# Performance work log

Hardware: AMD Instinct MI355X
Metric: run time of the kernel (lower is better)

Reference implementation:

```python
import jax, jax.numpy as jnp
import numpy as np

B, D, H, T = 8192, 256, 266, 20  # batch, dim, dim+10, num timesteps
LAMBDA = 1.0
SIGMA = 1.0
EPS = 1e-5  # torch BatchNorm1d default eps


def _bn(h, g, b):
    # training-mode BatchNorm1d: biased batch statistics over axis 0
    m = h.mean(0)
    v = h.var(0)
    return g * (h - m) * jax.lax.rsqrt(v + EPS) + b


def _hidden(x, W, b, g, be):
    return jax.nn.relu(_bn(x @ W.T + b, g, be))


def setup_inputs() -> dict:
    key = jax.random.key(0)
    ks = jax.random.split(key, 16)

    def n(k, shape, s=0.05):
        return jax.random.normal(k, shape, jnp.float32) * s

    inp = {}
    inp["x"] = jax.random.normal(ks[0], (B, D), jnp.float32)
    inp["xi"] = jax.random.normal(ks[1], (T, B, D), jnp.float32)
    inp["timegrid"] = jnp.linspace(0.0, 1.0, T + 1).astype(jnp.float32)
    # per-timestep stacks of Linear+BN params (i_h1, h1_h2, h2_o)
    inp["W1"] = n(ks[2], (T, H, D)); inp["b1"] = jnp.zeros((T, H), jnp.float32)
    inp["g1"] = jnp.ones((T, H), jnp.float32); inp["be1"] = jnp.zeros((T, H), jnp.float32)
    inp["W2"] = n(ks[3], (T, H, H)); inp["b2"] = jnp.zeros((T, H), jnp.float32)
    inp["g2"] = jnp.ones((T, H), jnp.float32); inp["be2"] = jnp.zeros((T, H), jnp.float32)
    inp["W3"] = n(ks[4], (T, D, H)); inp["b3"] = jnp.zeros((T, D), jnp.float32)
    # v0 network: hiddenLayer(D,H) -> hiddenLayer(H,H) -> hiddenLayer(H,1)
    inp["vW1"] = n(ks[5], (H, D)); inp["vb1"] = jnp.zeros((H,), jnp.float32)
    inp["vg1"] = jnp.ones((H,), jnp.float32); inp["vbe1"] = jnp.zeros((H,), jnp.float32)
    inp["vW2"] = n(ks[6], (H, H)); inp["vb2"] = jnp.zeros((H,), jnp.float32)
    inp["vg2"] = jnp.ones((H,), jnp.float32); inp["vbe2"] = jnp.zeros((H,), jnp.float32)
    inp["vW3"] = n(ks[7], (1, H)); inp["vb3"] = jnp.zeros((1,), jnp.float32)
    inp["vg3"] = jnp.ones((1,), jnp.float32); inp["vbe3"] = jnp.zeros((1,), jnp.float32)
    return inp


def reference(x, xi, timegrid, W1, b1, g1, be1, W2, b2, g2, be2, W3, b3,
              vW1, vb1, vg1, vbe1, vW2, vb2, vg2, vbe2, vW3, vb3, vg3, vbe3):
    # v0 sub-network evaluated on the initial x (i == 0 branch)
    v0 = _hidden(x, vW1, vb1, vg1, vbe1)
    v0 = _hidden(v0, vW2, vb2, vg2, vbe2)
    v0 = _hidden(v0, vW3, vb3, vg3, vbe3)  # [B, 1]

    hsteps = timegrid[1:] - timegrid[:-1]  # [T]

    def step(carry, inp_t):
        xt, vt = carry
        (W1t, b1t, g1t, be1t, W2t, b2t, g2t, be2t, W3t, b3t, ht, xit) = inp_t
        h1 = _hidden(xt, W1t, b1t, g1t, be1t)
        h2 = _hidden(h1, W2t, b2t, g2t, be2t)
        grad = h2 @ W3t.T + b3t                     # [B, D]
        alpha = -jnp.sqrt(LAMBDA) * grad
        f = jnp.sum(alpha * alpha, axis=1)          # ||alpha||_2^2 per row
        noise = SIGMA * jnp.sqrt(ht) * xit          # sigma*sqrt(h)*xi
        # diag(grad @ noise.T) == row-wise dot product (same math, O(B*D))
        dot = jnp.sum(grad * noise, axis=1)
        vt = vt - (f * ht)[:, None] + dot[:, None]
        xt = xt + alpha * ht + noise
        return (xt, vt), None

    (xT, vT), _ = jax.lax.scan(
        step, (x, v0),
        (W1, b1, g1, be1, W2, b2, g2, be2, W3, b3, hsteps, xi))
    return vT, xT
```

## Files before the change

kernel.cpp:

```cpp
#include <hip/hip_runtime.h>
#include <hip/hip_bf16.h>
#include <math.h>

#define BATCH 8192
#define DDIM 256
#define HDIM 266
#define NPAD 320
#define TSTEPS 20
#define BN_EPS 1e-5f
#define LSTR 72

typedef __attribute__((ext_vector_type(8))) short short8;
typedef __attribute__((ext_vector_type(4))) float f32x4;

__device__ __forceinline__ short f2bf(float f) {
    __hip_bfloat16 h = __float2bfloat16(f);
    return *reinterpret_cast<short*>(&h);
}
__device__ __forceinline__ float bf2f(short s) {
    union { unsigned u; float f; } v;
    v.u = ((unsigned)(unsigned short)s) << 16;
    return v.f;
}

#define SZ_W1B (20L * 320 * 256)
#define SZ_W2B (20L * 320 * 320)
#define SZ_W3B (20L * 256 * 320)
#define SZ_VW1 (320L * 256)
#define SZ_VW2 (320L * 320)
#define SZ_B1P (20L * 320)
#define SZ_B2P (20L * 320)
#define PREP_TOTAL (SZ_W1B + SZ_W2B + SZ_W3B + SZ_VW1 + SZ_VW2 + SZ_B1P + SZ_B2P + 3 * 320)

__global__ __launch_bounds__(256)
void prep_k(short* __restrict__ W1b, const float* __restrict__ W1,
            short* __restrict__ W2b, const float* __restrict__ W2,
            short* __restrict__ W3b, const float* __restrict__ W3,
            short* __restrict__ vW1b, const float* __restrict__ vW1,
            short* __restrict__ vW2b, const float* __restrict__ vW2,
            float* __restrict__ b1p, const float* __restrict__ b1,
            float* __restrict__ b2p, const float* __restrict__ b2,
            float* __restrict__ vb1p, const float* __restrict__ vb1,
            float* __restrict__ vb2p, const float* __restrict__ vb2,
            float* __restrict__ vW3p, const float* __restrict__ vW3)
{
    long idx = (long)blockIdx.x * 256 + threadIdx.x;
    if (idx < SZ_W1B) {
        long k = idx % 256, r = (idx / 256) % 320, t = idx / (256L * 320);
        float v = (r < HDIM) ? W1[((size_t)t * HDIM + r) * 256 + k] : 0.0f;
        W1b[idx] = f2bf(v); return;
    }
    idx -= SZ_W1B;
    if (idx < SZ_W2B) {
        long k = idx % 320, r = (idx / 320) % 320, t = idx / (320L * 320);
        float v = (r < HDIM && k < HDIM) ? W2[((size_t)t * HDIM + r) * HDIM + k] : 0.0f;
        W2b[idx] = f2bf(v); return;
    }
    idx -= SZ_W2B;
    if (idx < SZ_W3B) {
        long k = idx % 320, r = (idx / 320) % 256, t = idx / (320L * 256);
        float v = (k < HDIM) ? W3[((size_t)t * 256 + r) * HDIM + k] : 0.0f;
        W3b[idx] = f2bf(v); return;
    }
    idx -= SZ_W3B;
    if (idx < SZ_VW1) {
        long k = idx % 256, r = idx / 256;
        float v = (r < HDIM) ? vW1[(size_t)r * 256 + k] : 0.0f;
        vW1b[idx] = f2bf(v); return;
    }
    idx -= SZ_VW1;
    if (idx < SZ_VW2) {
        long k = idx % 320, r = idx / 320;
        float v = (r < HDIM && k < HDIM) ? vW2[(size_t)r * HDIM + k] : 0.0f;
        vW2b[idx] = f2bf(v); return;
    }
    idx -= SZ_VW2;
    if (idx < SZ_B1P) { long n = idx % 320, t = idx / 320;
        b1p[idx] = (n < HDIM) ? b1[(size_t)t * HDIM + n] : 0.0f; return; }
    idx -= SZ_B1P;
    if (idx < SZ_B2P) { long n = idx % 320, t = idx / 320;
        b2p[idx] = (n < HDIM) ? b2[(size_t)t * HDIM + n] : 0.0f; return; }
    idx -= SZ_B2P;
    if (idx < 320) { vb1p[idx] = (idx < HDIM) ? vb1[idx] : 0.0f; return; }
    idx -= 320;
    if (idx < 320) { vb2p[idx] = (idx < HDIM) ? vb2[idx] : 0.0f; return; }
    idx -= 320;
    if (idx < 320) { vW3p[idx] = (idx < HDIM) ? vW3[idx] : 0.0f; return; }
}

__global__ __launch_bounds__(256)
void init_k(const float* __restrict__ x, short* __restrict__ xtb,
            float* __restrict__ zbase, int zcount)
{
    int i = blockIdx.x * 256 + threadIdx.x;
    if (i < BATCH * DDIM) xtb[i] = f2bf(x[i]);
    if (i < zcount) zbase[i] = 0.0f;
}

__global__ __launch_bounds__(256)
void gemm1_k(const short* __restrict__ A, const short* __restrict__ W,
             const float* __restrict__ biasp, short* __restrict__ C,
             float* __restrict__ csum, float* __restrict__ csq)
{
    __shared__ __align__(16) short As[64 * LSTR];
    __shared__ __align__(16) short Bs[64 * LSTR];
    const int tid = threadIdx.x;
    const int col0 = blockIdx.x * 64, row0 = blockIdx.y * 64;
    const int lane = tid & 63, w = tid >> 6, q = lane >> 4, m = lane & 15;
    const int wr = (w >> 1) * 32, wc = (w & 1) * 32;
    const int srow = tid >> 2, kq = (tid & 3) * 8;

    const short* ap = A + (size_t)(row0 + srow) * DDIM + kq;
    const short* wp = W + (size_t)(col0 + srow) * DDIM + kq;
    short8 ra0 = *(const short8*)ap;
    short8 ra1 = *(const short8*)(ap + 32);
    short8 rw0 = *(const short8*)wp;
    short8 rw1 = *(const short8*)(wp + 32);

    f32x4 acc[2][2];
    #pragma unroll
    for (int i = 0; i < 2; ++i)
        #pragma unroll
        for (int j = 0; j < 2; ++j) acc[i][j] = (f32x4){0.f, 0.f, 0.f, 0.f};

    #pragma unroll
    for (int kt = 0; kt < 4; ++kt) {
        *(short8*)&As[srow * LSTR + kq]      = ra0;
        *(short8*)&As[srow * LSTR + kq + 32] = ra1;
        *(short8*)&Bs[srow * LSTR + kq]      = rw0;
        *(short8*)&Bs[srow * LSTR + kq + 32] = rw1;
        __syncthreads();
        if (kt < 3) {
            ap += 64; wp += 64;
            ra0 = *(const short8*)ap; ra1 = *(const short8*)(ap + 32);
            rw0 = *(const short8*)wp; rw1 = *(const short8*)(wp + 32);
        }
        #pragma unroll
        for (int kk = 0; kk < 2; ++kk) {
            short8 fa0 = *(const short8*)&As[(wr + m)      * LSTR + kk * 32 + q * 8];
            short8 fa1 = *(const short8*)&As[(wr + 16 + m) * LSTR + kk * 32 + q * 8];
            short8 fb0 = *(const short8*)&Bs[(wc + m)      * LSTR + kk * 32 + q * 8];
            short8 fb1 = *(const short8*)&Bs[(wc + 16 + m) * LSTR + kk * 32 + q * 8];
            acc[0][0] = __builtin_amdgcn_mfma_f32_16x16x32_bf16(fa0, fb0, acc[0][0], 0, 0, 0);
            acc[0][1] = __builtin_amdgcn_mfma_f32_16x16x32_bf16(fa0, fb1, acc[0][1], 0, 0, 0);
            acc[1][0] = __builtin_amdgcn_mfma_f32_16x16x32_bf16(fa1, fb0, acc[1][0], 0, 0, 0);
            acc[1][1] = __builtin_amdgcn_mfma_f32_16x16x32_bf16(fa1, fb1, acc[1][1], 0, 0, 0);
        }
        __syncthreads();
    }

    float cs[2], cq[2];
    #pragma unroll
    for (int j = 0; j < 2; ++j) {
        const int col = col0 + wc + j * 16 + m;
        const float bv = biasp[col];
        float s = 0.0f, sq = 0.0f;
        #pragma unroll
        for (int i = 0; i < 2; ++i)
            #pragma unroll
            for (int r = 0; r < 4; ++r) {
                float v = acc[i][j][r] + bv;
                int row = row0 + wr + i * 16 + q * 4 + r;
                C[(size_t)row * NPAD + col] = f2bf(v);
                s += v; sq += v * v;
            }
        cs[j] = s; cq[j] = sq;
    }
    #pragma unroll
    for (int j = 0; j < 2; ++j) {
        cs[j] += __shfl_xor(cs[j], 16); cs[j] += __shfl_xor(cs[j], 32);
        cq[j] += __shfl_xor(cq[j], 16); cq[j] += __shfl_xor(cq[j], 32);
    }
    float* reds = (float*)As;
    float* redq = (float*)Bs;
    if (q == 0) {
        #pragma unroll
        for (int j = 0; j < 2; ++j) {
            reds[(w >> 1) * 64 + wc + j * 16 + m] = cs[j];
            redq[(w >> 1) * 64 + wc + j * 16 + m] = cq[j];
        }
    }
    __syncthreads();
    if (tid < 64) {
        int col = col0 + tid;
        if (col < HDIM) {
            atomicAdd(&csum[col], reds[tid] + reds[64 + tid]);
            atomicAdd(&csq[col],  redq[tid] + redq[64 + tid]);
        }
    }
}

__global__ __launch_bounds__(256)
void gemm2_k(const short* __restrict__ A, const short* __restrict__ W,
             const float* __restrict__ biasp,
             const float* __restrict__ csum_in, const float* __restrict__ csq_in,
             const float* __restrict__ g, const float* __restrict__ be,
             short* __restrict__ C,
             float* __restrict__ csum_out, float* __restrict__ csq_out)
{
    __shared__ __align__(16) short As[32 * LSTR];
    __shared__ __align__(16) short Bs[160 * LSTR];
    __shared__ float sS[NPAD], sT[NPAD];
    const int tid = threadIdx.x;
    for (int k = tid; k < NPAD; k += 256) {
        float s = 0.0f, t = 0.0f;
        if (k < HDIM) {
            float mn = csum_in[k] * (1.0f / BATCH);
            float vr = csq_in[k] * (1.0f / BATCH) - mn * mn;
            float rs = rsqrtf(fmaxf(vr, 0.0f) + BN_EPS);
            s = g[k] * rs;
            t = be[k] - mn * s;
        }
        sS[k] = s; sT[k] = t;
    }
    __syncthreads();

    const int col0 = blockIdx.x * 160, row0 = blockIdx.y * 32;
    const int lane = tid & 63, w = tid >> 6, q = lane >> 4, m = lane & 15;
    const int rh = w >> 1, ch = w & 1;
    const int srowA = tid >> 3, kqA = (tid & 7) * 8;

    const short* ap = A + (size_t)(row0 + srowA) * NPAD + kqA;
    short8 rA = *(const short8*)ap;
    short8 rB[5];
    #pragma unroll
    for (int i = 0; i < 5; ++i) {
        int s = tid + 256 * i;
        rB[i] = *(const short8*)(W + (size_t)(col0 + (s >> 3)) * NPAD + ((s & 7) * 8));
    }

    f32x4 acc[5];
    #pragma unroll
    for (int j = 0; j < 5; ++j) acc[j] = (f32x4){0.f, 0.f, 0.f, 0.f};

    #pragma unroll
    for (int kt = 0; kt < 5; ++kt) {
        short8 ta;
        const int kb = kt * 64 + kqA;
        #pragma unroll
        for (int j = 0; j < 8; ++j) {
            float f = bf2f(rA[j]);
            f = fmaxf(f * sS[kb + j] + sT[kb + j], 0.0f);
            ta[j] = f2bf(f);
        }
        *(short8*)&As[srowA * LSTR + kqA] = ta;
        #pragma unroll
        for (int i = 0; i < 5; ++i) {
            int s = tid + 256 * i;
            *(short8*)&Bs[(s >> 3) * LSTR + (s & 7) * 8] = rB[i];
        }
        __syncthreads();
        if (kt < 4) {
            ap += 64;
            rA = *(const short8*)ap;
            #pragma unroll
            for (int i = 0; i < 5; ++i) {
                int s = tid + 256 * i;
                rB[i] = *(const short8*)(W + (size_t)(col0 + (s >> 3)) * NPAD
                                         + (kt + 1) * 64 + ((s & 7) * 8));
            }
        }
        #pragma unroll
        for (int kk = 0; kk < 2; ++kk) {
            short8 fa = *(const short8*)&As[(rh * 16 + m) * LSTR + kk * 32 + q * 8];
            #pragma unroll
            for (int j = 0; j < 5; ++j) {
                short8 fb = *(const short8*)&Bs[(ch * 80 + j * 16 + m) * LSTR + kk * 32 + q * 8];
                acc[j] = __builtin_amdgcn_mfma_f32_16x16x32_bf16(fa, fb, acc[j], 0, 0, 0);
            }
        }
        __syncthreads();
    }

    float csv[5], cqv[5];
    #pragma unroll
    for (int j = 0; j < 5; ++j) {
        const int col = col0 + ch * 80 + j * 16 + m;
        const float bv = biasp[col];
        float s = 0.0f, sq = 0.0f;
        #pragma unroll
        for (int r = 0; r < 4; ++r) {
            float v = acc[j][r] + bv;
            int row = row0 + rh * 16 + q * 4 + r;
            C[(size_t)row * NPAD + col] = f2bf(v);
            s += v; sq += v * v;
        }
        csv[j] = s; cqv[j] = sq;
    }
    #pragma unroll
    for (int j = 0; j < 5; ++j) {
        csv[j] += __shfl_xor(csv[j], 16); csv[j] += __shfl_xor(csv[j], 32);
        cqv[j] += __shfl_xor(cqv[j], 16); cqv[j] += __shfl_xor(cqv[j], 32);
    }
    float* redS = (float*)As;
    float* redQ = redS + 320;
    if (q == 0) {
        #pragma unroll
        for (int j = 0; j < 5; ++j) {
            redS[rh * 160 + ch * 80 + j * 16 + m] = csv[j];
            redQ[rh * 160 + ch * 80 + j * 16 + m] = cqv[j];
        }
    }
    __syncthreads();
    if (tid < 160) {
        int col = col0 + tid;
        if (col < HDIM) {
            atomicAdd(&csum_out[col], redS[tid] + redS[160 + tid]);
            atomicAdd(&csq_out[col],  redQ[tid] + redQ[160 + tid]);
        }
    }
}

__global__ __launch_bounds__(256)
void gemm3_k(const short* __restrict__ A, const short* __restrict__ W,
             const float* __restrict__ bias,
             const float* __restrict__ csum_in, const float* __restrict__ csq_in,
             const float* __restrict__ g, const float* __restrict__ be,
             const float* __restrict__ xi_t,
             short* __restrict__ xtb, float* __restrict__ xout,
             float* __restrict__ ftab, float* __restrict__ dtab,
             const float* __restrict__ tg, int t, int last)
{
    __shared__ __align__(16) short As[32 * LSTR];
    __shared__ __align__(16) short Bs[128 * LSTR];
    __shared__ float sS[NPAD], sT[NPAD];
    const int tid = threadIdx.x;
    for (int k = tid; k < NPAD; k += 256) {
        float s = 0.0f, tt = 0.0f;
        if (k < HDIM) {
            float mn = csum_in[k] * (1.0f / BATCH);
            float vr = csq_in[k] * (1.0f / BATCH) - mn * mn;
            float rs = rsqrtf(fmaxf(vr, 0.0f) + BN_EPS);
            s = g[k] * rs;
            tt = be[k] - mn * s;
        }
        sS[k] = s; sT[k] = tt;
    }
    __syncthreads();

    const int col0 = blockIdx.x * 128, row0 = blockIdx.y * 32;
    const int lane = tid & 63, w = tid >> 6, q = lane >> 4, m = lane & 15;
    const int rh = w >> 1, ch = w & 1;
    const int srowA = tid >> 3, kqA = (tid & 7) * 8;

    const short* ap = A + (size_t)(row0 + srowA) * NPAD + kqA;
    short8 rA = *(const short8*)ap;
    short8 rB[4];
    #pragma unroll
    for (int i = 0; i < 4; ++i) {
        int s = tid + 256 * i;
        rB[i] = *(const short8*)(W + (size_t)(col0 + (s >> 3)) * NPAD + ((s & 7) * 8));
    }

    f32x4 acc[4];
    #pragma unroll
    for (int j = 0; j < 4; ++j) acc[j] = (f32x4){0.f, 0.f, 0.f, 0.f};

    #pragma unroll
    for (int kt = 0; kt < 5; ++kt) {
        short8 ta;
        const int kb = kt * 64 + kqA;
        #pragma unroll
        for (int j = 0; j < 8; ++j) {
            float f = bf2f(rA[j]);
            f = fmaxf(f * sS[kb + j] + sT[kb + j], 0.0f);
            ta[j] = f2bf(f);
        }
        *(short8*)&As[srowA * LSTR + kqA] = ta;
        #pragma unroll
        for (int i = 0; i < 4; ++i) {
            int s = tid + 256 * i;
            *(short8*)&Bs[(s >> 3) * LSTR + (s & 7) * 8] = rB[i];
        }
        __syncthreads();
        if (kt < 4) {
            ap += 64;
            rA = *(const short8*)ap;
            #pragma unroll
            for (int i = 0; i < 4; ++i) {
                int s = tid + 256 * i;
                rB[i] = *(const short8*)(W + (size_t)(col0 + (s >> 3)) * NPAD
                                         + (kt + 1) * 64 + ((s & 7) * 8));
            }
        }
        #pragma unroll
        for (int kk = 0; kk < 2; ++kk) {
            short8 fa = *(const short8*)&As[(rh * 16 + m) * LSTR + kk * 32 + q * 8];
            #pragma unroll
            for (int j = 0; j < 4; ++j) {
                short8 fb = *(const short8*)&Bs[(ch * 64 + j * 16 + m) * LSTR + kk * 32 + q * 8];
                acc[j] = __builtin_amdgcn_mfma_f32_16x16x32_bf16(fa, fb, acc[j], 0, 0, 0);
            }
        }
        __syncthreads();
    }

    const float ht = tg[t + 1] - tg[t];
    const float sn = sqrtf(ht);
    float fr[4] = {0.f, 0.f, 0.f, 0.f};
    float dr[4] = {0.f, 0.f, 0.f, 0.f};
    #pragma unroll
    for (int j = 0; j < 4; ++j) {
        const int col = col0 + ch * 64 + j * 16 + m;
        const float bv = bias[col];
        #pragma unroll
        for (int r = 0; r < 4; ++r) {
            const int row = row0 + rh * 16 + q * 4 + r;
            size_t idx = (size_t)row * DDIM + col;
            float grad = acc[j][r] + bv;
            float noise = sn * xi_t[idx];
            float nx = bf2f(xtb[idx]) - grad * ht + noise;
            xtb[idx] = f2bf(nx);
            if (last) xout[idx] = nx;
            fr[r] += grad * grad;
            dr[r] += grad * noise;
        }
    }
    #pragma unroll
    for (int r = 0; r < 4; ++r) {
        fr[r] += __shfl_xor(fr[r], 1); dr[r] += __shfl_xor(dr[r], 1);
        fr[r] += __shfl_xor(fr[r], 2); dr[r] += __shfl_xor(dr[r], 2);
        fr[r] += __shfl_xor(fr[r], 4); dr[r] += __shfl_xor(dr[r], 4);
        fr[r] += __shfl_xor(fr[r], 8); dr[r] += __shfl_xor(dr[r], 8);
    }
    if (m == 0) {
        #pragma unroll
        for (int r = 0; r < 4; ++r) {
            const int row = row0 + rh * 16 + q * 4 + r;
            atomicAdd(&ftab[row], fr[r]);
            atomicAdd(&dtab[row], dr[r]);
        }
    }
}

__global__ __launch_bounds__(256)
void vrow_k(const short* __restrict__ A,
            const float* __restrict__ csum_in, const float* __restrict__ csq_in,
            const float* __restrict__ g, const float* __restrict__ be,
            const float* __restrict__ vW3p, const float* __restrict__ vb3,
            float* __restrict__ pre3, float* __restrict__ s3, float* __restrict__ q3)
{
    __shared__ float sS[NPAD], sT[NPAD];
    __shared__ float wred[8];
    const int tid = threadIdx.x;
    for (int k = tid; k < NPAD; k += 256) {
        float s = 0.0f, t = 0.0f;
        if (k < HDIM) {
            float mn = csum_in[k] * (1.0f / BATCH);
            float vr = csq_in[k] * (1.0f / BATCH) - mn * mn;
            float rs = rsqrtf(fmaxf(vr, 0.0f) + BN_EPS);
            s = g[k] * rs;
            t = be[k] - mn * s;
        }
        sS[k] = s; sT[k] = t;
    }
    __syncthreads();
    const int wave = tid >> 6, lane = tid & 63;
    const int row = blockIdx.x * 4 + wave;
    float sum = 0.0f;
    #pragma unroll
    for (int c = 0; c < 5; ++c) {
        int k = c * 64 + lane;
        float v = fmaxf(bf2f(A[(size_t)row * NPAD + k]) * sS[k] + sT[k], 0.0f);
        sum += v * vW3p[k];
    }
    sum += __shfl_xor(sum, 1);  sum += __shfl_xor(sum, 2);
    sum += __shfl_xor(sum, 4);  sum += __shfl_xor(sum, 8);
    sum += __shfl_xor(sum, 16); sum += __shfl_xor(sum, 32);
    if (lane == 0) {
        float p = sum + vb3[0];
        pre3[row] = p;
        wred[wave] = p;
        wred[4 + wave] = p * p;
    }
    __syncthreads();
    if (tid == 0) {
        atomicAdd(s3, wred[0] + wred[1] + wred[2] + wred[3]);
        atomicAdd(q3, wred[4] + wred[5] + wred[6] + wred[7]);
    }
}

__global__ __launch_bounds__(256)
void v3b_k(const float* __restrict__ pre3,
           const float* __restrict__ s3, const float* __restrict__ q3,
           const float* __restrict__ vg3, const float* __restrict__ vbe3,
           float* __restrict__ vt)
{
    int i = blockIdx.x * 256 + threadIdx.x;
    float mn = s3[0] * (1.0f / BATCH);
    float va = fmaxf(q3[0] * (1.0f / BATCH) - mn * mn, 0.0f);
    float rs = rsqrtf(va + BN_EPS);
    if (i < BATCH) vt[i] = fmaxf(vg3[0] * (pre3[i] - mn) * rs + vbe3[0], 0.0f);
}

__global__ __launch_bounds__(256)
void final_v_k(const float* __restrict__ vt,
               const float* __restrict__ ftab, const float* __restrict__ dtab,
               const float* __restrict__ tg, float* __restrict__ outv)
{
    int i = blockIdx.x * 256 + threadIdx.x;
    if (i >= BATCH) return;
    float v = vt[i];
    for (int t = 0; t < TSTEPS; ++t) {
        float ht = tg[t + 1] - tg[t];
        v += dtab[(size_t)t * BATCH + i] - ftab[(size_t)t * BATCH + i] * ht;
    }
    outv[i] = v;
}

extern "C" void kernel_launch(void* const* d_in, const int* in_sizes, int n_in,
                              void* d_out, int out_size, void* d_ws, size_t ws_size,
                              hipStream_t stream)
{
    const float* x    = (const float*)d_in[0];
    const float* xi   = (const float*)d_in[1];
    const float* tg   = (const float*)d_in[2];
    const float* W1   = (const float*)d_in[3];
    const float* b1   = (const float*)d_in[4];
    const float* g1   = (const float*)d_in[5];
    const float* be1  = (const float*)d_in[6];
    const float* W2   = (const float*)d_in[7];
    const float* b2   = (const float*)d_in[8];
    const float* g2   = (const float*)d_in[9];
    const float* be2  = (const float*)d_in[10];
    const float* W3   = (const float*)d_in[11];
    const float* b3   = (const float*)d_in[12];
    const float* vW1  = (const float*)d_in[13];
    const float* vb1  = (const float*)d_in[14];
    const float* vg1  = (const float*)d_in[15];
    const float* vbe1 = (const float*)d_in[16];
    const float* vW2  = (const float*)d_in[17];
    const float* vb2  = (const float*)d_in[18];
    const float* vg2  = (const float*)d_in[19];
    const float* vbe2 = (const float*)d_in[20];
    const float* vW3  = (const float*)d_in[21];
    const float* vb3  = (const float*)d_in[22];
    const float* vg3  = (const float*)d_in[23];
    const float* vbe3 = (const float*)d_in[24];

    float* out  = (float*)d_out;
    float* xout = out + BATCH;

    short* xtb  = (short*)d_ws;
    short* hp1  = xtb + (size_t)BATCH * DDIM;
    short* hp2  = hp1 + (size_t)BATCH * NPAD;
    short* W1b  = hp2 + (size_t)BATCH * NPAD;
    short* W2b  = W1b + SZ_W1B;
    short* W3b  = W2b + SZ_W2B;
    short* vW1b = W3b + SZ_W3B;
    short* vW2b = vW1b + SZ_VW1;
    float* fbase = (float*)(vW2b + SZ_VW2);
    float* b1p  = fbase;
    float* b2p  = b1p + TSTEPS * NPAD;
    float* vb1p = b2p + TSTEPS * NPAD;
    float* vb2p = vb1p + NPAD;
    float* vW3p = vb2p + NPAD;
    float* vt   = vW3p + NPAD;
    float* pre3 = vt + BATCH;
    float* ftab = pre3 + BATCH;
    float* dtab = ftab + (size_t)TSTEPS * BATCH;
    float* csA  = dtab + (size_t)TSTEPS * BATCH;
    float* cqA  = csA + 21 * NPAD;
    float* csB  = cqA + 21 * NPAD;
    float* cqB  = csB + 21 * NPAD;
    float* s3   = cqB + 21 * NPAD;
    float* q3   = s3 + 1;
    const int zcount = 2 * TSTEPS * BATCH + 4 * 21 * NPAD + 2;

    dim3 blk(256);
    dim3 g1g(5, BATCH / 64);
    dim3 g2g(2, BATCH / 32);
    dim3 g3g(2, BATCH / 32);

    init_k<<<dim3((BATCH * DDIM + 255) / 256), blk, 0, stream>>>(x, xtb, ftab, zcount);
    prep_k<<<dim3((int)((PREP_TOTAL + 255) / 256)), blk, 0, stream>>>(
        W1b, W1, W2b, W2, W3b, W3, vW1b, vW1, vW2b, vW2,
        b1p, b1, b2p, b2, vb1p, vb1, vb2p, vb2, vW3p, vW3);

    float* csV1 = csA + 20 * NPAD; float* cqV1 = cqA + 20 * NPAD;
    float* csV2 = csB + 20 * NPAD; float* cqV2 = cqB + 20 * NPAD;
    gemm1_k<<<g1g, blk, 0, stream>>>(xtb, vW1b, vb1p, hp1, csV1, cqV1);
    gemm2_k<<<g2g, blk, 0, stream>>>(hp1, vW2b, vb2p, csV1, cqV1, vg1, vbe1,
                                     hp2, csV2, cqV2);
    vrow_k<<<dim3(BATCH / 4), blk, 0, stream>>>(hp2, csV2, cqV2, vg2, vbe2,
                                                vW3p, vb3, pre3, s3, q3);
    v3b_k<<<dim3(BATCH / 256), blk, 0, stream>>>(pre3, s3, q3, vg3, vbe3, vt);

    for (int t = 0; t < TSTEPS; ++t) {
        gemm1_k<<<g1g, blk, 0, stream>>>(
            xtb, W1b + (size_t)t * NPAD * DDIM, b1p + t * NPAD,
            hp1, csA + t * NPAD, cqA + t * NPAD);
        gemm2_k<<<g2g, blk, 0, stream>>>(
            hp1, W2b + (size_t)t * NPAD * NPAD, b2p + t * NPAD,
            csA + t * NPAD, cqA + t * NPAD, g1 + t * HDIM, be1 + t * HDIM,
            hp2, csB + t * NPAD, cqB + t * NPAD);
        gemm3_k<<<g3g, blk, 0, stream>>>(
            hp2, W3b + (size_t)t * DDIM * NPAD, b3 + t * DDIM,
            csB + t * NPAD, cqB + t * NPAD, g2 + t * HDIM, be2 + t * HDIM,
            xi + (size_t)t * BATCH * DDIM, xtb, xout,
            ftab + (size_t)t * BATCH, dtab + (size_t)t * BATCH,
            tg, t, (t == TSTEPS - 1) ? 1 : 0);
    }
    final_v_k<<<dim3(BATCH / 256), blk, 0, stream>>>(vt, ftab, dtab, tg, out);
}
```

Before: 1.144 ms.

## Fuse next-step first-layer GEMM into output GEMM and batch v0 network launches

Gemm3 now produces full 32-row tiles across all 256 output columns with 512-thread blocks, so each block can immediately run the next timestep's first-layer GEMM on its freshly updated x rows from shared memory. This removes the per-step gemm1 launch and its re-read of xt. The v0 network runs alongside step 0 through a z-dimension of the grid, and init and the v3b work are merged into prep and the final kernel. ftab/dtab are written directly rather than by atomics. The trade-off is larger shared memory and register use per block and fewer blocks in flight (256 blocks), which may lower occupancy.

```diff
diff --git a/kernel.cpp b/kernel.cpp
--- a/kernel.cpp
+++ b/kernel.cpp
@@ -30,7 +30,9 @@
 #define SZ_VW2 (320L * 320)
 #define SZ_B1P (20L * 320)
 #define SZ_B2P (20L * 320)
-#define PREP_TOTAL (SZ_W1B + SZ_W2B + SZ_W3B + SZ_VW1 + SZ_VW2 + SZ_B1P + SZ_B2P + 3 * 320)
+#define SZ_XTB (8192L * 256)
+#define ZCOUNT (4L * 21 * NPAD + 2)
+#define PREP_TOTAL (SZ_W1B + SZ_W2B + SZ_W3B + SZ_VW1 + SZ_VW2 + SZ_B1P + SZ_B2P + 3 * 320 + SZ_XTB + ZCOUNT)
 
 __global__ __launch_bounds__(256)
 void prep_k(short* __restrict__ W1b, const float* __restrict__ W1,
@@ -42,7 +44,9 @@
             float* __restrict__ b2p, const float* __restrict__ b2,
             float* __restrict__ vb1p, const float* __restrict__ vb1,
             float* __restrict__ vb2p, const float* __restrict__ vb2,
-            float* __restrict__ vW3p, const float* __restrict__ vW3)
+            float* __restrict__ vW3p, const float* __restrict__ vW3,
+            const float* __restrict__ x, short* __restrict__ xtb,
+            float* __restrict__ zbase)
 {
     long idx = (long)blockIdx.x * 256 + threadIdx.x;
     if (idx < SZ_W1B) {
@@ -86,22 +90,25 @@
     if (idx < 320) { vb2p[idx] = (idx < HDIM) ? vb2[idx] : 0.0f; return; }
     idx -= 320;
     if (idx < 320) { vW3p[idx] = (idx < HDIM) ? vW3[idx] : 0.0f; return; }
+    idx -= 320;
+    if (idx < SZ_XTB) { xtb[idx] = f2bf(x[idx]); return; }
+    idx -= SZ_XTB;
+    if (idx < ZCOUNT) { zbase[idx] = 0.0f; return; }
 }
 
 __global__ __launch_bounds__(256)
-void init_k(const float* __restrict__ x, short* __restrict__ xtb,
-            float* __restrict__ zbase, int zcount)
+void gemm1_k(const short* __restrict__ A,
+             const short* __restrict__ W0a, const float* __restrict__ bias0,
+             short* __restrict__ C0a, float* __restrict__ cs0, float* __restrict__ cq0,
+             const short* __restrict__ W1a, const float* __restrict__ bias1,
+             short* __restrict__ C1a, float* __restrict__ cs1, float* __restrict__ cq1)
 {
-    int i = blockIdx.x * 256 + threadIdx.x;
-    if (i < BATCH * DDIM) xtb[i] = f2bf(x[i]);
-    if (i < zcount) zbase[i] = 0.0f;
-}
-
-__global__ __launch_bounds__(256)
-void gemm1_k(const short* __restrict__ A, const short* __restrict__ W,
-             const float* __restrict__ biasp, short* __restrict__ C,
-             float* __restrict__ csum, float* __restrict__ csq)
-{
+    const short* W      = blockIdx.z ? W1a   : W0a;
+    const float* biasp  = blockIdx.z ? bias1 : bias0;
+    short* C            = blockIdx.z ? C1a   : C0a;
+    float* csum         = blockIdx.z ? cs1   : cs0;
+    float* csq          = blockIdx.z ? cq1   : cq0;
+
     __shared__ __align__(16) short As[64 * LSTR];
     __shared__ __align__(16) short Bs[64 * LSTR];
     const int tid = threadIdx.x;
@@ -191,13 +198,28 @@
 }
 
 __global__ __launch_bounds__(256)
-void gemm2_k(const short* __restrict__ A, const short* __restrict__ W,
-             const float* __restrict__ biasp,
-             const float* __restrict__ csum_in, const float* __restrict__ csq_in,
-             const float* __restrict__ g, const float* __restrict__ be,
-             short* __restrict__ C,
-             float* __restrict__ csum_out, float* __restrict__ csq_out)
+void gemm2_k(const short* __restrict__ A0a, const short* __restrict__ W0a,
+             const float* __restrict__ bias0,
+             const float* __restrict__ csi0, const float* __restrict__ cqi0,
+             const float* __restrict__ g0a, const float* __restrict__ be0a,
+             short* __restrict__ C0a, float* __restrict__ cso0, float* __restrict__ cqo0,
+             const short* __restrict__ A1a, const short* __restrict__ W1a,
+             const float* __restrict__ bias1,
+             const float* __restrict__ csi1, const float* __restrict__ cqi1,
+             const float* __restrict__ g1a, const float* __restrict__ be1a,
+             short* __restrict__ C1a, float* __restrict__ cso1, float* __restrict__ cqo1)
 {
+    const short* A       = blockIdx.z ? A1a   : A0a;
+    const short* W       = blockIdx.z ? W1a   : W0a;
+    const float* biasp   = blockIdx.z ? bias1 : bias0;
+    const float* csum_in = blockIdx.z ? csi1  : csi0;
+    const float* csq_in  = blockIdx.z ? cqi1  : cqi0;
+    const float* g       = blockIdx.z ? g1a   : g0a;
+    const float* be      = blockIdx.z ? be1a  : be0a;
+    short* C             = blockIdx.z ? C1a   : C0a;
+    float* csum_out      = blockIdx.z ? cso1  : cso0;
+    float* csq_out       = blockIdx.z ? cqo1  : cqo0;
+
     __shared__ __align__(16) short As[32 * LSTR];
     __shared__ __align__(16) short Bs[160 * LSTR];
     __shared__ float sS[NPAD], sT[NPAD];
@@ -311,21 +333,78 @@
     }
 }
 
-__global__ __launch_bounds__(256)
-void gemm3_k(const short* __restrict__ A, const short* __restrict__ W,
-             const float* __restrict__ bias,
-             const float* __restrict__ csum_in, const float* __restrict__ csq_in,
-             const float* __restrict__ g, const float* __restrict__ be,
-             const float* __restrict__ xi_t,
-             short* __restrict__ xtb, float* __restrict__ xout,
-             float* __restrict__ ftab, float* __restrict__ dtab,
-             const float* __restrict__ tg, int t, int last)
+__global__ __launch_bounds__(512)
+void g31_k(const short* __restrict__ A,
+           const short* __restrict__ W3t, const float* __restrict__ b3t,
+           const float* __restrict__ csum_in, const float* __restrict__ csq_in,
+           const float* __restrict__ g, const float* __restrict__ be,
+           const float* __restrict__ xi_t,
+           short* __restrict__ xtb, float* __restrict__ xout,
+           float* __restrict__ ftab_t, float* __restrict__ dtab_t,
+           const float* __restrict__ tg, int t, int last,
+           const short* __restrict__ W1n, const float* __restrict__ b1n,
+           short* __restrict__ hp1, float* __restrict__ csn, float* __restrict__ cqn,
+           const short* __restrict__ Av, const float* __restrict__ csV, const float* __restrict__ cqV,
+           const float* __restrict__ vg, const float* __restrict__ vbe,
+           const float* __restrict__ vW3p, const float* __restrict__ vb3,
+           float* __restrict__ pre3, float* __restrict__ s3, float* __restrict__ q3)
 {
-    __shared__ __align__(16) short As[32 * LSTR];
-    __shared__ __align__(16) short Bs[128 * LSTR];
+    __shared__ __align__(16) short As1[32 * LSTR];
+    __shared__ __align__(16) short As2[128 * LSTR];
+    __shared__ __align__(16) short Bs[320 * LSTR];
     __shared__ float sS[NPAD], sT[NPAD];
+    __shared__ float redF[128], redD[128];
+    __shared__ float redS[2 * NPAD], redQ[2 * NPAD];
+
     const int tid = threadIdx.x;
-    for (int k = tid; k < NPAD; k += 256) {
+    const int row0 = blockIdx.x * 32;
+
+    if (blockIdx.z == 1) {
+        for (int k = tid; k < NPAD; k += 512) {
+            float s = 0.0f, tt = 0.0f;
+            if (k < HDIM) {
+                float mn = csV[k] * (1.0f / BATCH);
+                float vr = cqV[k] * (1.0f / BATCH) - mn * mn;
+                float rs = rsqrtf(fmaxf(vr, 0.0f) + BN_EPS);
+                s = vg[k] * rs;
+                tt = vbe[k] - mn * s;
+            }
+            sS[k] = s; sT[k] = tt;
+        }
+        __syncthreads();
+        const int wv = tid >> 6, lane = tid & 63;
+        float ps = 0.0f, pq = 0.0f;
+        #pragma unroll
+        for (int r4 = 0; r4 < 4; ++r4) {
+            int row = row0 + wv * 4 + r4;
+            float sum = 0.0f;
+            #pragma unroll
+            for (int c = 0; c < 5; ++c) {
+                int k = c * 64 + lane;
+                float v = fmaxf(bf2f(Av[(size_t)row * NPAD + k]) * sS[k] + sT[k], 0.0f);
+                sum += v * vW3p[k];
+            }
+            sum += __shfl_xor(sum, 1);  sum += __shfl_xor(sum, 2);
+            sum += __shfl_xor(sum, 4);  sum += __shfl_xor(sum, 8);
+            sum += __shfl_xor(sum, 16); sum += __shfl_xor(sum, 32);
+            if (lane == 0) {
+                float p = sum + vb3[0];
+                pre3[row] = p;
+                ps += p; pq += p * p;
+            }
+        }
+        if (lane == 0) { redF[wv] = ps; redD[wv] = pq; }
+        __syncthreads();
+        if (tid == 0) {
+            float a = 0.0f, b = 0.0f;
+            #pragma unroll
+            for (int i = 0; i < 8; ++i) { a += redF[i]; b += redD[i]; }
+            atomicAdd(s3, a); atomicAdd(q3, b);
+        }
+        return;
+    }
+
+    for (int k = tid; k < NPAD; k += 512) {
         float s = 0.0f, tt = 0.0f;
         if (k < HDIM) {
             float mn = csum_in[k] * (1.0f / BATCH);
@@ -338,18 +417,18 @@
     }
     __syncthreads();
 
-    const int col0 = blockIdx.x * 128, row0 = blockIdx.y * 32;
     const int lane = tid & 63, w = tid >> 6, q = lane >> 4, m = lane & 15;
-    const int rh = w >> 1, ch = w & 1;
+    const int rh = w >> 2, ch = w & 3;
     const int srowA = tid >> 3, kqA = (tid & 7) * 8;
 
     const short* ap = A + (size_t)(row0 + srowA) * NPAD + kqA;
-    short8 rA = *(const short8*)ap;
+    short8 rA;
+    if (tid < 256) rA = *(const short8*)ap;
     short8 rB[4];
     #pragma unroll
     for (int i = 0; i < 4; ++i) {
-        int s = tid + 256 * i;
-        rB[i] = *(const short8*)(W + (size_t)(col0 + (s >> 3)) * NPAD + ((s & 7) * 8));
+        int s = tid + 512 * i;
+        rB[i] = *(const short8*)(W3t + (size_t)(s >> 3) * NPAD + ((s & 7) * 8));
     }
 
     f32x4 acc[4];
@@ -358,34 +437,36 @@
 
     #pragma unroll
     for (int kt = 0; kt < 5; ++kt) {
-        short8 ta;
-        const int kb = kt * 64 + kqA;
-        #pragma unroll
-        for (int j = 0; j < 8; ++j) {
-            float f = bf2f(rA[j]);
-            f = fmaxf(f * sS[kb + j] + sT[kb + j], 0.0f);
-            ta[j] = f2bf(f);
-        }
-        *(short8*)&As[srowA * LSTR + kqA] = ta;
+        if (tid < 256) {
+            short8 ta;
+            const int kb = kt * 64 + kqA;
+            #pragma unroll
+            for (int j = 0; j < 8; ++j) {
+                float f = bf2f(rA[j]);
+                f = fmaxf(f * sS[kb + j] + sT[kb + j], 0.0f);
+                ta[j] = f2bf(f);
+            }
+            *(short8*)&As1[srowA * LSTR + kqA] = ta;
+        }
         #pragma unroll
         for (int i = 0; i < 4; ++i) {
-            int s = tid + 256 * i;
+            int s = tid + 512 * i;
             *(short8*)&Bs[(s >> 3) * LSTR + (s & 7) * 8] = rB[i];
         }
         __syncthreads();
         if (kt < 4) {
             ap += 64;
-            rA = *(const short8*)ap;
+            if (tid < 256) rA = *(const short8*)ap;
             #pragma unroll
             for (int i = 0; i < 4; ++i) {
-                int s = tid + 256 * i;
-                rB[i] = *(const short8*)(W + (size_t)(col0 + (s >> 3)) * NPAD
+                int s = tid + 512 * i;
+                rB[i] = *(const short8*)(W3t + (size_t)(s >> 3) * NPAD
                                          + (kt + 1) * 64 + ((s & 7) * 8));
             }
         }
         #pragma unroll
         for (int kk = 0; kk < 2; ++kk) {
-            short8 fa = *(const short8*)&As[(rh * 16 + m) * LSTR + kk * 32 + q * 8];
+            short8 fa = *(const short8*)&As1[(rh * 16 + m) * LSTR + kk * 32 + q * 8];
             #pragma unroll
             for (int j = 0; j < 4; ++j) {
                 short8 fb = *(const short8*)&Bs[(ch * 64 + j * 16 + m) * LSTR + kk * 32 + q * 8];
@@ -393,6 +474,15 @@
             }
         }
         __syncthreads();
+    }
+
+    short8 rW[5];
+    if (!last) {
+        #pragma unroll
+        for (int i = 0; i < 5; ++i) {
+            int s = tid + 512 * i;
+            rW[i] = *(const short8*)(W1n + (size_t)(s >> 3) * DDIM + ((s & 7) * 8));
+        }
     }
 
     const float ht = tg[t + 1] - tg[t];
@@ -401,17 +491,18 @@
     float dr[4] = {0.f, 0.f, 0.f, 0.f};
     #pragma unroll
     for (int j = 0; j < 4; ++j) {
-        const int col = col0 + ch * 64 + j * 16 + m;
-        const float bv = bias[col];
+        const int col = ch * 64 + j * 16 + m;
+        const float bv = b3t[col];
         #pragma unroll
         for (int r = 0; r < 4; ++r) {
-            const int row = row0 + rh * 16 + q * 4 + r;
-            size_t idx = (size_t)row * DDIM + col;
+            const int lr = rh * 16 + q * 4 + r;
+            const size_t idx = (size_t)(row0 + lr) * DDIM + col;
             float grad = acc[j][r] + bv;
             float noise = sn * xi_t[idx];
             float nx = bf2f(xtb[idx]) - grad * ht + noise;
             xtb[idx] = f2bf(nx);
             if (last) xout[idx] = nx;
+            else      As2[(ch * 32 + lr) * LSTR + (j * 16 + m)] = f2bf(nx);
             fr[r] += grad * grad;
             dr[r] += grad * noise;
         }
@@ -426,81 +517,96 @@
     if (m == 0) {
         #pragma unroll
         for (int r = 0; r < 4; ++r) {
-            const int row = row0 + rh * 16 + q * 4 + r;
-            atomicAdd(&ftab[row], fr[r]);
-            atomicAdd(&dtab[row], dr[r]);
-        }
+            redF[ch * 32 + rh * 16 + q * 4 + r] = fr[r];
+            redD[ch * 32 + rh * 16 + q * 4 + r] = dr[r];
+        }
+    }
+    __syncthreads();
+    if (tid < 32) {
+        ftab_t[row0 + tid] = redF[tid] + redF[32 + tid] + redF[64 + tid] + redF[96 + tid];
+        dtab_t[row0 + tid] = redD[tid] + redD[32 + tid] + redD[64 + tid] + redD[96 + tid];
+    }
+    if (last) return;
+
+    f32x4 acc2[5];
+    #pragma unroll
+    for (int j = 0; j < 5; ++j) acc2[j] = (f32x4){0.f, 0.f, 0.f, 0.f};
+
+    #pragma unroll
+    for (int kt = 0; kt < 4; ++kt) {
+        #pragma unroll
+        for (int i = 0; i < 5; ++i) {
+            int s = tid + 512 * i;
+            *(short8*)&Bs[(s >> 3) * LSTR + (s & 7) * 8] = rW[i];
+        }
+        __syncthreads();
+        if (kt < 3) {
+            #pragma unroll
+            for (int i = 0; i < 5; ++i) {
+                int s = tid + 512 * i;
+                rW[i] = *(const short8*)(W1n + (size_t)(s >> 3) * DDIM
+                                         + (kt + 1) * 64 + ((s & 7) * 8));
+            }
+        }
+        #pragma unroll
+        for (int kk = 0; kk < 2; ++kk) {
+            short8 fa = *(const short8*)&As2[(kt * 32 + rh * 16 + m) * LSTR + kk * 32 + q * 8];
+            #pragma unroll
+            for (int j = 0; j < 5; ++j) {
+                short8 fb = *(const short8*)&Bs[(ch * 80 + j * 16 + m) * LSTR + kk * 32 + q * 8];
+                acc2[j] = __builtin_amdgcn_mfma_f32_16x16x32_bf16(fa, fb, acc2[j], 0, 0, 0);
+            }
+        }
+        __syncthreads();
+    }
+
+    float csv[5], cqv[5];
+    #pragma unroll
+    for (int j = 0; j < 5; ++j) {
+        const int col = ch * 80 + j * 16 + m;
+        const float bv = b1n[col];
+        float s = 0.0f, sq = 0.0f;
+        #pragma unroll
+        for (int r = 0; r < 4; ++r) {
+            float v = acc2[j][r] + bv;
+            int row = row0 + rh * 16 + q * 4 + r;
+            hp1[(size_t)row * NPAD + col] = f2bf(v);
+            s += v; sq += v * v;
+        }
+        csv[j] = s; cqv[j] = sq;
+    }
+    #pragma unroll
+    for (int j = 0; j < 5; ++j) {
+        csv[j] += __shfl_xor(csv[j], 16); csv[j] += __shfl_xor(csv[j], 32);
+        cqv[j] += __shfl_xor(cqv[j], 16); cqv[j] += __shfl_xor(cqv[j], 32);
+    }
+    if (q == 0) {
+        #pragma unroll
+        for (int j = 0; j < 5; ++j) {
+            redS[rh * NPAD + ch * 80 + j * 16 + m] = csv[j];
+            redQ[rh * NPAD + ch * 80 + j * 16 + m] = cqv[j];
+        }
+    }
+    __syncthreads();
+    if (tid < HDIM) {
+        atomicAdd(&csn[tid], redS[tid] + redS[NPAD + tid]);
+        atomicAdd(&cqn[tid], redQ[tid] + redQ[NPAD + tid]);
     }
 }
 
 __global__ __launch_bounds__(256)
-void vrow_k(const short* __restrict__ A,
-            const float* __restrict__ csum_in, const float* __restrict__ csq_in,
-            const float* __restrict__ g, const float* __restrict__ be,
-            const float* __restrict__ vW3p, const float* __restrict__ vb3,
-            float* __restrict__ pre3, float* __restrict__ s3, float* __restrict__ q3)
-{
-    __shared__ float sS[NPAD], sT[NPAD];
-    __shared__ float wred[8];
-    const int tid = threadIdx.x;
-    for (int k = tid; k < NPAD; k += 256) {
-        float s = 0.0f, t = 0.0f;
-        if (k < HDIM) {
-            float mn = csum_in[k] * (1.0f / BATCH);
-            float vr = csq_in[k] * (1.0f / BATCH) - mn * mn;
-            float rs = rsqrtf(fmaxf(vr, 0.0f) + BN_EPS);
-            s = g[k] * rs;
-            t = be[k] - mn * s;
-        }
-        sS[k] = s; sT[k] = t;
-    }
-    __syncthreads();
-    const int wave = tid >> 6, lane = tid & 63;
-    const int row = blockIdx.x * 4 + wave;
-    float sum = 0.0f;
-    #pragma unroll
-    for (int c = 0; c < 5; ++c) {
-        int k = c * 64 + lane;
-        float v = fmaxf(bf2f(A[(size_t)row * NPAD + k]) * sS[k] + sT[k], 0.0f);
-        sum += v * vW3p[k];
-    }
-    sum += __shfl_xor(sum, 1);  sum += __shfl_xor(sum, 2);
-    sum += __shfl_xor(sum, 4);  sum += __shfl_xor(sum, 8);
-    sum += __shfl_xor(sum, 16); sum += __shfl_xor(sum, 32);
-    if (lane == 0) {
-        float p = sum + vb3[0];
-        pre3[row] = p;
-        wred[wave] = p;
-        wred[4 + wave] = p * p;
-    }
-    __syncthreads();
-    if (tid == 0) {
-        atomicAdd(s3, wred[0] + wred[1] + wred[2] + wred[3]);
-        atomicAdd(q3, wred[4] + wred[5] + wred[6] + wred[7]);
-    }
-}
-
-__global__ __launch_bounds__(256)
-void v3b_k(const float* __restrict__ pre3,
-           const float* __restrict__ s3, const float* __restrict__ q3,
-           const float* __restrict__ vg3, const float* __restrict__ vbe3,
-           float* __restrict__ vt)
-{
-    int i = blockIdx.x * 256 + threadIdx.x;
-    float mn = s3[0] * (1.0f / BATCH);
-    float va = fmaxf(q3[0] * (1.0f / BATCH) - mn * mn, 0.0f);
-    float rs = rsqrtf(va + BN_EPS);
-    if (i < BATCH) vt[i] = fmaxf(vg3[0] * (pre3[i] - mn) * rs + vbe3[0], 0.0f);
-}
-
-__global__ __launch_bounds__(256)
-void final_v_k(const float* __restrict__ vt,
+void final_v_k(const float* __restrict__ pre3,
+               const float* __restrict__ s3, const float* __restrict__ q3,
+               const float* __restrict__ vg3, const float* __restrict__ vbe3,
                const float* __restrict__ ftab, const float* __restrict__ dtab,
                const float* __restrict__ tg, float* __restrict__ outv)
 {
     int i = blockIdx.x * 256 + threadIdx.x;
     if (i >= BATCH) return;
-    float v = vt[i];
+    float mn = s3[0] * (1.0f / BATCH);
+    float va = fmaxf(q3[0] * (1.0f / BATCH) - mn * mn, 0.0f);
+    float rs = rsqrtf(va + BN_EPS);
+    float v = fmaxf(vg3[0] * (pre3[i] - mn) * rs + vbe3[0], 0.0f);
     for (int t = 0; t < TSTEPS; ++t) {
         float ht = tg[t + 1] - tg[t];
         v += dtab[(size_t)t * BATCH + i] - ftab[(size_t)t * BATCH + i] * ht;
@@ -544,7 +650,9 @@
     short* xtb  = (short*)d_ws;
     short* hp1  = xtb + (size_t)BATCH * DDIM;
     short* hp2  = hp1 + (size_t)BATCH * NPAD;
-    short* W1b  = hp2 + (size_t)BATCH * NPAD;
+    short* hp1v = hp2 + (size_t)BATCH * NPAD;
+    short* hp2v = hp1v + (size_t)BATCH * NPAD;
+    short* W1b  = hp2v + (size_t)BATCH * NPAD;
     short* W2b  = W1b + SZ_W1B;
     short* W3b  = W2b + SZ_W2B;
     short* vW1b = W3b + SZ_W3B;
@@ -555,8 +663,7 @@
     float* vb1p = b2p + TSTEPS * NPAD;
     float* vb2p = vb1p + NPAD;
     float* vW3p = vb2p + NPAD;
-    float* vt   = vW3p + NPAD;
-    float* pre3 = vt + BATCH;
+    float* pre3 = vW3p + NPAD;
     float* ftab = pre3 + BATCH;
     float* dtab = ftab + (size_t)TSTEPS * BATCH;
     float* csA  = dtab + (size_t)TSTEPS * BATCH;
@@ -565,41 +672,45 @@
     float* cqB  = csB + 21 * NPAD;
     float* s3   = cqB + 21 * NPAD;
     float* q3   = s3 + 1;
-    const int zcount = 2 * TSTEPS * BATCH + 4 * 21 * NPAD + 2;
-
-    dim3 blk(256);
-    dim3 g1g(5, BATCH / 64);
-    dim3 g2g(2, BATCH / 32);
-    dim3 g3g(2, BATCH / 32);
-
-    init_k<<<dim3((BATCH * DDIM + 255) / 256), blk, 0, stream>>>(x, xtb, ftab, zcount);
+
+    float* csV1 = csA + 20 * NPAD; float* cqV1 = cqA + 20 * NPAD;
+    float* csV2 = csB + 20 * NPAD; float* cqV2 = cqB + 20 * NPAD;
+
+    dim3 blk(256), blk5(512);
+
     prep_k<<<dim3((int)((PREP_TOTAL + 255) / 256)), blk, 0, stream>>>(
         W1b, W1, W2b, W2, W3b, W3, vW1b, vW1, vW2b, vW2,
-        b1p, b1, b2p, b2, vb1p, vb1, vb2p, vb2, vW3p, vW3);
-
-    float* csV1 = csA + 20 * NPAD; float* cqV1 = cqA + 20 * NPAD;
-    float* csV2 = csB + 20 * NPAD; float* cqV2 = cqB + 20 * NPAD;
-    gemm1_k<<<g1g, blk, 0, stream>>>(xtb, vW1b, vb1p, hp1, csV1, cqV1);
-    gemm2_k<<<g2g, blk, 0, stream>>>(hp1, vW2b, vb2p, csV1, cqV1, vg1, vbe1,
-                                     hp2, csV2, cqV2);
-    vrow_k<<<dim3(BATCH / 4), blk, 0, stream>>>(hp2, csV2, cqV2, vg2, vbe2,
-                                                vW3p, vb3, pre3, s3, q3);
-    v3b_k<<<dim3(BATCH / 256), blk, 0, stream>>>(pre3, s3, q3, vg3, vbe3, vt);
+        b1p, b1, b2p, b2, vb1p, vb1, vb2p, vb2, vW3p, vW3,
+        x, xtb, csA);
+
+    gemm1_k<<<dim3(5, BATCH / 64, 2), blk, 0, stream>>>(
+        xtb, W1b, b1p, hp1, csA, cqA,
+        vW1b, vb1p, hp1v, csV1, cqV1);
+    gemm2_k<<<dim3(2, BATCH / 32, 2), blk, 0, stream>>>(
+        hp1, W2b, b2p, csA, cqA, g1, be1, hp2, csB, cqB,
+        hp1v, vW2b, vb2p, csV1, cqV1, vg1, vbe1, hp2v, csV2, cqV2);
 
     for (int t = 0; t < TSTEPS; ++t) {
-        gemm1_k<<<g1g, blk, 0, stream>>>(
-            xtb, W1b + (size_t)t * NPAD * DDIM, b1p + t * NPAD,
-            hp1, csA + t * NPAD, cqA + t * NPAD);
-        gemm2_k<<<g2g, blk, 0, stream>>>(
-            hp1, W2b + (size_t)t * NPAD * NPAD, b2p + t * NPAD,
-            csA + t * NPAD, cqA + t * NPAD, g1 + t * HDIM, be1 + t * HDIM,
-            hp2, csB + t * NPAD, cqB + t * NPAD);
-        gemm3_k<<<g3g, blk, 0, stream>>>(
+        if (t > 0)
+            gemm2_k<<<dim3(2, BATCH / 32, 1), blk, 0, stream>>>(
+                hp1, W2b + (size_t)t * NPAD * NPAD, b2p + t * NPAD,
+                csA + t * NPAD, cqA + t * NPAD, g1 + t * HDIM, be1 + t * HDIM,
+                hp2, csB + t * NPAD, cqB + t * NPAD,
+                nullptr, nullptr, nullptr, nullptr, nullptr,
+                nullptr, nullptr, nullptr, nullptr, nullptr);
+        const int last = (t == TSTEPS - 1) ? 1 : 0;
+        const int tn = last ? 0 : t + 1;
+        g31_k<<<dim3(BATCH / 32, 1, (t == 0) ? 2 : 1), blk5, 0, stream>>>(
             hp2, W3b + (size_t)t * DDIM * NPAD, b3 + t * DDIM,
             csB + t * NPAD, cqB + t * NPAD, g2 + t * HDIM, be2 + t * HDIM,
             xi + (size_t)t * BATCH * DDIM, xtb, xout,
             ftab + (size_t)t * BATCH, dtab + (size_t)t * BATCH,
-            tg, t, (t == TSTEPS - 1) ? 1 : 0);
-    }
-    final_v_k<<<dim3(BATCH / 256), blk, 0, stream>>>(vt, ftab, dtab, tg, out);
+            tg, t, last,
+            W1b + (size_t)tn * NPAD * DDIM, b1p + tn * NPAD,
+            hp1, csA + tn * NPAD, cqA + tn * NPAD,
+            hp2v, csV2, cqV2, vg2, vbe2, vW3p, vb3, pre3, s3, q3);
+    }
+
+    final_v_k<<<dim3(BATCH / 256), blk, 0, stream>>>(
+        pre3, s3, q3, vg3, vbe3, ftab, dtab, tg, out);
 }
```

Measured after the change: 1.107 ms. -3.2%, faster.
